# Optimization experiments

Hardware: AMD Instinct MI355X
Metric: run time of the kernel (lower is better)

Reference implementation:

```python
import jax, jax.numpy as jnp
from jax import lax
import numpy as np

B, T, F = 64, 2048, 256
H0, H1, O = 512, 512, 128


def setup_inputs() -> dict:
    key = jax.random.key(0)
    ks = jax.random.split(key, 16)
    s = lambda n: 1.0 / np.sqrt(n)
    return {
        "x": jax.random.normal(ks[0], (B, T, F), dtype=jnp.float32),
        # layer 0 RNN params (torch nn.RNN layout: W_ih [H,F], W_hh [H,H])
        "W_ih0": jax.random.uniform(ks[1], (H0, F), jnp.float32, -s(H0), s(H0)),
        "W_hh0": jax.random.uniform(ks[2], (H0, H0), jnp.float32, -s(H0), s(H0)),
        "b_ih0": jax.random.uniform(ks[3], (H0,), jnp.float32, -s(H0), s(H0)),
        "b_hh0": jax.random.uniform(ks[4], (H0,), jnp.float32, -s(H0), s(H0)),
        "h0_0": jax.random.normal(ks[5], (H0,), dtype=jnp.float32),  # buffer layer1 [1,1,H0]
        # layer 1 RNN params
        "W_ih1": jax.random.uniform(ks[6], (H1, H0), jnp.float32, -s(H1), s(H1)),
        "W_hh1": jax.random.uniform(ks[7], (H1, H1), jnp.float32, -s(H1), s(H1)),
        "b_ih1": jax.random.uniform(ks[8], (H1,), jnp.float32, -s(H1), s(H1)),
        "b_hh1": jax.random.uniform(ks[9], (H1,), jnp.float32, -s(H1), s(H1)),
        "h0_1": jax.random.normal(ks[10], (H1,), dtype=jnp.float32),  # buffer layer2 [1,1,H1]
        # final linear head
        "W_fc": jax.random.uniform(ks[11], (O, H1), jnp.float32, -s(H1), s(H1)),
        "b_fc": jax.random.uniform(ks[12], (O,), jnp.float32, -s(H1), s(H1)),
    }


def _rnn_layer(x, W_ih, W_hh, b_ih, b_hh, h0):
    # x: [B, T, Fin]; returns (outputs [B, T, H], last hidden [B, H])
    bs = x.shape[0]
    # precompute input projection as one big GEMM: [B, T, H]
    xp = jnp.einsum("btf,hf->bth", x, W_ih) + b_ih + b_hh
    h_init = jnp.broadcast_to(h0, (bs, h0.shape[0]))

    def step(h, xp_t):  # h: [B, H], xp_t: [B, H]
        h_new = jnp.tanh(xp_t + h @ W_hh.T)
        return h_new, h_new

    hT, hs = lax.scan(step, h_init, xp.transpose(1, 0, 2))  # time-major scan
    return hs.transpose(1, 0, 2), hT


def reference(x, W_ih0, W_hh0, b_ih0, b_hh0, h0_0,
              W_ih1, W_hh1, b_ih1, b_hh1, h0_1, W_fc, b_fc):
    res, _ = _rnn_layer(x, W_ih0, W_hh0, b_ih0, b_hh0, h0_0)
    _, hT = _rnn_layer(res, W_ih1, W_hh1, b_ih1, b_hh1, h0_1)
    # op[-1] is the last layer's final hidden state: [B, H1]
    return hT @ W_fc.T + b_fc  # [B, O]
```

## Files before the change

### kernel.cpp

```cpp
#include <hip/hip_runtime.h>

typedef _Float16 half_t;
typedef _Float16 f16x2 __attribute__((ext_vector_type(2)));
typedef _Float16 f16x8 __attribute__((ext_vector_type(8)));
typedef float f32x4 __attribute__((ext_vector_type(4)));

#define B_SZ 64
#define T_SZ 2048
#define F_SZ 256
#define H_SZ 512
#define O_SZ 128
#define NCH 32
#define CH 64

#if defined(__has_builtin)
#if __has_builtin(__builtin_amdgcn_fdot2)
#define HAS_FDOT2 1
#endif
#if __has_builtin(__builtin_amdgcn_rcpf)
#define HAS_RCPF 1
#endif
#endif
#ifndef HAS_FDOT2
#define HAS_FDOT2 0
#endif
#ifndef HAS_RCPF
#define HAS_RCPF 0
#endif

static __device__ __forceinline__ float fdot2(unsigned int w, unsigned int h, float acc) {
#if HAS_FDOT2
    return __builtin_amdgcn_fdot2(__builtin_bit_cast(f16x2, w), __builtin_bit_cast(f16x2, h), acc, false);
#else
    f16x2 wv = __builtin_bit_cast(f16x2, w);
    f16x2 hv = __builtin_bit_cast(f16x2, h);
    return acc + (float)wv[0] * (float)hv[0] + (float)wv[1] * (float)hv[1];
#endif
}

static __device__ __forceinline__ unsigned int pack_pair(float a, float b) {
    f16x2 p;
    p[0] = (half_t)a;
    p[1] = (half_t)b;
    return __builtin_bit_cast(unsigned int, p);
}

static __device__ __forceinline__ float fast_rcp(float x) {
#if HAS_RCPF
    return __builtin_amdgcn_rcpf(x);
#else
    return 1.0f / x;
#endif
}

static __device__ __forceinline__ void step_barrier() {
    __builtin_amdgcn_sched_barrier(0);
    asm volatile("s_waitcnt lgkmcnt(0)" ::: "memory");
    __builtin_amdgcn_s_barrier();
    __builtin_amdgcn_sched_barrier(0);
}


__global__ void cvt_f32_f16(const float* __restrict__ src, half_t* __restrict__ dst, int n) {
    int i = blockIdx.x * 256 + threadIdx.x;
    if (i < n) dst[i] = (half_t)src[i];
}

__global__ void zero_flags(unsigned int* __restrict__ p, int n) {
    int i = blockIdx.x * 256 + threadIdx.x;
    if (i < n) p[i] = 0u;
}

template<bool A_F32, int K>
__global__ __launch_bounds__(256) void gemm_xp(const void* __restrict__ Aptr,
                                               const half_t* __restrict__ Bw,
                                               const float* __restrict__ bias1,
                                               const float* __restrict__ bias2,
                                               half_t* __restrict__ Cout)
{
    const int nt   = blockIdx.x & 7;
    const int mt   = blockIdx.x >> 3;
    const int wave = threadIdx.x >> 6;
    const int lane = threadIdx.x & 63;
    const int mrow = mt * 64 + wave * 16 + (lane & 15);
    const int koff = (lane >> 4) * 8;

    f32x4 acc[4];
#pragma unroll
    for (int i = 0; i < 4; i++) acc[i] = (f32x4){0.f, 0.f, 0.f, 0.f};

#pragma unroll 2
    for (int k0 = 0; k0 < K; k0 += 32) {
        f16x8 a;
        if (A_F32) {
            const float* ap = (const float*)Aptr + (size_t)mrow * K + (k0 + koff);
            float4 v0 = ((const float4*)ap)[0];
            float4 v1 = ((const float4*)ap)[1];
            a[0] = (half_t)v0.x; a[1] = (half_t)v0.y; a[2] = (half_t)v0.z; a[3] = (half_t)v0.w;
            a[4] = (half_t)v1.x; a[5] = (half_t)v1.y; a[6] = (half_t)v1.z; a[7] = (half_t)v1.w;
        } else {
            const half_t* ap = (const half_t*)Aptr + (size_t)mrow * K + (k0 + koff);
            a = *(const f16x8*)ap;
        }
#pragma unroll
        for (int cb = 0; cb < 4; cb++) {
            const int col = nt * 64 + cb * 16 + (lane & 15);
            f16x8 bfrag = *(const f16x8*)(Bw + (size_t)col * K + (k0 + koff));
            acc[cb] = __builtin_amdgcn_mfma_f32_16x16x32_f16(a, bfrag, acc[cb], 0, 0, 0);
        }
    }
    const int rbase = mt * 64 + wave * 16 + (lane >> 4) * 4;
#pragma unroll
    for (int cb = 0; cb < 4; cb++) {
        const int col = nt * 64 + cb * 16 + (lane & 15);
        const float bsum = bias1[col] + bias2[col];
#pragma unroll
        for (int r = 0; r < 4; r++) {
            Cout[(size_t)(rbase + r) * H_SZ + col] = (half_t)(acc[cb][r] + bsum);
        }
    }
}

__global__ __launch_bounds__(512, 2)
void rnn_mega(half_t* bufA, half_t* bufB,
              const float* __restrict__ Whh0, const float* __restrict__ Whh1,
              const half_t* __restrict__ Wih1h,
              const float* __restrict__ h0_0, const float* __restrict__ h0_1,
              const float* __restrict__ b_ih1, const float* __restrict__ b_hh1,
              float* hT,
              unsigned int* flags0, unsigned int* flags1)
{
    __shared__ __align__(16) float part[2][8 * H_SZ];
    __shared__ __align__(16) uint4 wlds[12 * 512];
    __shared__ __align__(16) half_t hbuf[H_SZ];

    const int role = blockIdx.x % 3;
    const int b    = blockIdx.x / 3;
    const int tid  = threadIdx.x;
    const int l    = tid & 63;
    const int s    = tid >> 6;

    if (role == 1) {
        const int w = s, lane = l;
        const int koff = (lane >> 4) * 8;
        for (int chunk = 0; chunk < NCH; chunk++) {
            if (tid == 0) {
                while (__hip_atomic_load(&flags0[b * NCH + chunk], __ATOMIC_ACQUIRE,
                                         __HIP_MEMORY_SCOPE_AGENT) == 0u)
                    __builtin_amdgcn_s_sleep(2);
            }
            __syncthreads();
            const int t0 = chunk * CH;

            f32x4 gac[4][4];
#pragma unroll
            for (int rt = 0; rt < 4; rt++)
#pragma unroll
                for (int cb = 0; cb < 4; cb++) gac[rt][cb] = (f32x4){0.f, 0.f, 0.f, 0.f};

#pragma unroll 1
            for (int k0 = 0; k0 < H_SZ; k0 += 32) {
                f16x8 bf[4];
#pragma unroll
                for (int cb = 0; cb < 4; cb++)
                    bf[cb] = *(const f16x8*)(Wih1h +
                              (size_t)(64 * w + 16 * cb + (lane & 15)) * H_SZ + k0 + koff);
#pragma unroll
                for (int rt = 0; rt < 4; rt++) {
                    const f16x8 a = *(const f16x8*)((const half_t*)bufA +
                              ((size_t)b * T_SZ + t0 + rt * 16 + (lane & 15)) * H_SZ + k0 + koff);
#pragma unroll
                    for (int cb = 0; cb < 4; cb++)
                        gac[rt][cb] = __builtin_amdgcn_mfma_f32_16x16x32_f16(a, bf[cb], gac[rt][cb], 0, 0, 0);
                }
            }
#pragma unroll
            for (int rt = 0; rt < 4; rt++) {
                const int rbase = t0 + rt * 16 + (lane >> 4) * 4;
#pragma unroll
                for (int cb = 0; cb < 4; cb++) {
                    const int col = 64 * w + 16 * cb + (lane & 15);
                    const float bsum = b_ih1[col] + b_hh1[col];
#pragma unroll
                    for (int r = 0; r < 4; r++)
                        bufB[((size_t)b * T_SZ + rbase + r) * H_SZ + col] =
                            (half_t)(gac[rt][cb][r] + bsum);
                }
            }
            __syncthreads();
            if (tid == 0)
                __hip_atomic_store(&flags1[b * NCH + chunk], 1u, __ATOMIC_RELEASE,
                                   __HIP_MEMORY_SCOPE_AGENT);
        }
        return;
    }

    const bool L1 = (role == 2);
    const float* Whh = L1 ? Whh1 : Whh0;

    unsigned int wreg[208];
#pragma unroll
    for (int r = 0; r < 8; r++) {
        const float* wrow = Whh + (size_t)(8 * l + r) * H_SZ + 64 * s;
#pragma unroll
        for (int c = 0; c < 26; c++)
            wreg[c * 8 + r] = pack_pair(wrow[2 * c], wrow[2 * c + 1]);
    }
#pragma unroll
    for (int p2 = 0; p2 < 6; p2++) {
#pragma unroll
        for (int rh = 0; rh < 2; rh++) {
            unsigned int q[4];
#pragma unroll
            for (int rr = 0; rr < 4; rr++) {
                const int r = rh * 4 + rr;
                const float* wrow = Whh + (size_t)(8 * l + r) * H_SZ + 64 * s;
                const int c = 26 + p2;
                q[rr] = pack_pair(wrow[2 * c], wrow[2 * c + 1]);
            }
            uint4 v;
            v.x = q[0]; v.y = q[1]; v.z = q[2]; v.w = q[3];
            wlds[(p2 * 2 + rh) * 512 + tid] = v;
        }
    }
    hbuf[tid] = (half_t)((L1 ? h0_1 : h0_0)[tid]);
    __syncthreads();

    unsigned short* xp16 = (unsigned short*)(L1 ? bufB : bufA);
    const size_t base = (size_t)b * T_SZ * H_SZ + tid;

    const uint4* h16 = (const uint4*)(hbuf + 64 * s);
    const int x1     = (l >> 2) & 1;
    const int pslot0 = s * 128 + 2 * l + x1;
    const int pslot1 = s * 128 + 2 * l + (x1 ^ 1);
    const int fbase  = ((2 * (tid >> 3) + (((tid >> 2) & 1) ^ ((tid >> 5) & 1))) << 2) | (tid & 3);

#pragma unroll 1
    for (int chunk = 0; chunk < NCH; chunk++) {
        const int t0 = chunk * CH;
        if (L1) {
            if (tid == 0) {
                while (__hip_atomic_load(&flags1[b * NCH + chunk], __ATOMIC_ACQUIRE,
                                         __HIP_MEMORY_SCOPE_AGENT) == 0u)
                    __builtin_amdgcn_s_sleep(2);
            }
            __syncthreads();
        }
        unsigned short xpw_next = xp16[base + (size_t)t0 * H_SZ];

#pragma unroll 1
        for (int tt = 0; tt < CH; tt++) {
            const int t = t0 + tt;
            const unsigned short xpw = xpw_next;
            if (tt + 1 < CH) xpw_next = xp16[base + (size_t)(t + 1) * H_SZ];

            float acc[8];
#pragma unroll
            for (int r = 0; r < 8; r++) acc[r] = 0.f;

#pragma unroll
            for (int cc = 0; cc < 6; cc++) {
                const uint4 hv = h16[cc];
                const unsigned int hx0 = hv.x, hx1 = hv.y, hx2 = hv.z, hx3 = hv.w;
#pragma unroll
                for (int r = 0; r < 8; r++) acc[r] = fdot2(wreg[(cc * 4 + 0) * 8 + r], hx0, acc[r]);
#pragma unroll
                for (int r = 0; r < 8; r++) acc[r] = fdot2(wreg[(cc * 4 + 1) * 8 + r], hx1, acc[r]);
#pragma unroll
                for (int r = 0; r < 8; r++) acc[r] = fdot2(wreg[(cc * 4 + 2) * 8 + r], hx2, acc[r]);
#pragma unroll
                for (int r = 0; r < 8; r++) acc[r] = fdot2(wreg[(cc * 4 + 3) * 8 + r], hx3, acc[r]);
            }
#define LDSP(P2, H2) { \
                const uint4 w0 = wlds[((P2) * 2 + 0) * 512 + tid]; \
                const uint4 w1 = wlds[((P2) * 2 + 1) * 512 + tid]; \
                acc[0] = fdot2(w0.x, (H2), acc[0]); acc[1] = fdot2(w0.y, (H2), acc[1]); \
                acc[2] = fdot2(w0.z, (H2), acc[2]); acc[3] = fdot2(w0.w, (H2), acc[3]); \
                acc[4] = fdot2(w1.x, (H2), acc[4]); acc[5] = fdot2(w1.y, (H2), acc[5]); \
                acc[6] = fdot2(w1.z, (H2), acc[6]); acc[7] = fdot2(w1.w, (H2), acc[7]); }
            {
                const uint4 hv6 = h16[6];
#pragma unroll
                for (int r = 0; r < 8; r++) acc[r] = fdot2(wreg[24 * 8 + r], hv6.x, acc[r]);
#pragma unroll
                for (int r = 0; r < 8; r++) acc[r] = fdot2(wreg[25 * 8 + r], hv6.y, acc[r]);
                LDSP(0, hv6.z)
                LDSP(1, hv6.w)
                const uint4 hv7 = h16[7];
                LDSP(2, hv7.x)
                LDSP(3, hv7.y)
                LDSP(4, hv7.z)
                LDSP(5, hv7.w)
            }
#undef LDSP

            const int par = tt & 1;
            {
                float4* pb = (float4*)&part[par][0];
                float4 p0, p1;
                p0.x = acc[0]; p0.y = acc[1]; p0.z = acc[2]; p0.w = acc[3];
                p1.x = acc[4]; p1.y = acc[5]; p1.z = acc[6]; p1.w = acc[7];
                pb[pslot0] = p0;
                pb[pslot1] = p1;
            }
            step_barrier();

            float y;
            {
                half_t xv = __builtin_bit_cast(half_t, xpw);
                y = (float)xv;
            }
#pragma unroll
            for (int s2 = 0; s2 < 8; s2++) y += part[par][s2 * 512 + fbase];

            float e  = __expf(2.0f * y);
            float hn = 1.0f - 2.0f * fast_rcp(e + 1.0f);
            hbuf[tid] = (half_t)hn;
            if (!L1)
                xp16[base + (size_t)t * H_SZ] = __builtin_bit_cast(unsigned short, (half_t)hn);
            else if (t == T_SZ - 1)
                hT[(size_t)b * H_SZ + tid] = hn;
        }
        if (!L1) {
            __syncthreads();
            if (tid == 0)
                __hip_atomic_store(&flags0[b * NCH + chunk], 1u, __ATOMIC_RELEASE,
                                   __HIP_MEMORY_SCOPE_AGENT);
        }
    }
}

__global__ __launch_bounds__(128) void head_fc(const float* __restrict__ hT,
                                               const float* __restrict__ Wfc,
                                               const float* __restrict__ bfc,
                                               float* __restrict__ out)
{
    __shared__ float hs[H_SZ];
    const int b = blockIdx.x, o = threadIdx.x;
    for (int i = o; i < H_SZ; i += 128) hs[i] = hT[(size_t)b * H_SZ + i];
    __syncthreads();
    const float4* w4 = (const float4*)(Wfc + (size_t)o * H_SZ);
    const float4* h4 = (const float4*)hs;
    float acc = 0.f;
#pragma unroll 4
    for (int k = 0; k < H_SZ / 4; k++) {
        float4 w = w4[k], h = h4[k];
        acc += w.x * h.x + w.y * h.y + w.z * h.z + w.w * h.w;
    }
    out[(size_t)b * O_SZ + o] = acc + bfc[o];
}


extern "C" void kernel_launch(void* const* d_in, const int* in_sizes, int n_in,
                              void* d_out, int out_size, void* d_ws, size_t ws_size,
                              hipStream_t stream) {
    const float* x     = (const float*)d_in[0];
    const float* W_ih0 = (const float*)d_in[1];
    const float* W_hh0 = (const float*)d_in[2];
    const float* b_ih0 = (const float*)d_in[3];
    const float* b_hh0 = (const float*)d_in[4];
    const float* h0_0  = (const float*)d_in[5];
    const float* W_ih1 = (const float*)d_in[6];
    const float* W_hh1 = (const float*)d_in[7];
    const float* b_ih1 = (const float*)d_in[8];
    const float* b_hh1 = (const float*)d_in[9];
    const float* h0_1  = (const float*)d_in[10];
    const float* W_fc  = (const float*)d_in[11];
    const float* b_fc  = (const float*)d_in[12];

    char* ws = (char*)d_ws;
    size_t off = 0;
    const size_t bufElems = (size_t)B_SZ * T_SZ * H_SZ;
    half_t* bufA  = (half_t*)(ws + off); off += bufElems * 2;
    half_t* bufB  = (half_t*)(ws + off); off += bufElems * 2;
    half_t* Wih0h = (half_t*)(ws + off); off += (size_t)H_SZ * F_SZ * 2;
    half_t* Wih1h = (half_t*)(ws + off); off += (size_t)H_SZ * H_SZ * 2;
    float*  hTbuf = (float*)(ws + off);  off += (size_t)B_SZ * H_SZ * 4;
    const int FLAG_N = B_SZ * NCH;
    unsigned int* flags0 = (unsigned int*)(ws + off); off += (size_t)FLAG_N * 4;
    unsigned int* flags1 = (unsigned int*)(ws + off); off += (size_t)FLAG_N * 4;

    const int M = B_SZ * T_SZ;

    zero_flags<<<(2 * FLAG_N + 255) / 256, 256, 0, stream>>>(flags0, 2 * FLAG_N);
    cvt_f32_f16<<<(H_SZ * F_SZ + 255) / 256, 256, 0, stream>>>(W_ih0, Wih0h, H_SZ * F_SZ);
    cvt_f32_f16<<<(H_SZ * H_SZ + 255) / 256, 256, 0, stream>>>(W_ih1, Wih1h, H_SZ * H_SZ);

    gemm_xp<true, F_SZ><<<(M / 64) * 8, 256, 0, stream>>>(x, Wih0h, b_ih0, b_hh0, bufA);

    rnn_mega<<<192, 512, 0, stream>>>(bufA, bufB, W_hh0, W_hh1, Wih1h,
                                      h0_0, h0_1, b_ih1, b_hh1,
                                      hTbuf, flags0, flags1);

    head_fc<<<B_SZ, 128, 0, stream>>>(hTbuf, W_fc, b_fc, (float*)d_out);
}
```

Measured before the change: 4.081 ms.

## Replace LDS partial-sum reduction with intra-wave DPP reduction and double-buffered h

Each wave now owns 64 output rows, and the K dimension is split across the 8 lanes of each lane-group. Partial dot products are combined with three DPP adds followed by a select tree, instead of being written to LDS and summed after the barrier. The hidden state moves to a padded, double-buffered LDS array, which removes the need for the part buffer and leaves one barrier per step. The cost is extra DPP and select instructions, and h reads that are spread across lanes instead of broadcast.

```diff
diff --git a/kernel.cpp b/kernel.cpp
--- a/kernel.cpp
+++ b/kernel.cpp
@@ -51,6 +51,12 @@
 #else
     return 1.0f / x;
 #endif
+}
+
+template<int CTRL>
+static __device__ __forceinline__ float dpp_add(float x) {
+    int y = __builtin_amdgcn_mov_dpp(__builtin_bit_cast(int, x), CTRL, 0xF, 0xF, true);
+    return x + __builtin_bit_cast(float, y);
 }
 
 static __device__ __forceinline__ void step_barrier() {
@@ -130,9 +136,8 @@
               float* hT,
               unsigned int* flags0, unsigned int* flags1)
 {
-    __shared__ __align__(16) float part[2][8 * H_SZ];
     __shared__ __align__(16) uint4 wlds[12 * 512];
-    __shared__ __align__(16) half_t hbuf[H_SZ];
+    __shared__ __align__(16) half_t hpad[2][8 * 72];
 
     const int role = blockIdx.x % 3;
     const int b    = blockIdx.x / 3;
@@ -198,10 +203,13 @@
     const bool L1 = (role == 2);
     const float* Whh = L1 ? Whh1 : Whh0;
 
+    const int q  = l >> 3;
+    const int sp = l & 7;
+
     unsigned int wreg[208];
 #pragma unroll
     for (int r = 0; r < 8; r++) {
-        const float* wrow = Whh + (size_t)(8 * l + r) * H_SZ + 64 * s;
+        const float* wrow = Whh + (size_t)(64 * s + 8 * q + r) * H_SZ + 64 * sp;
 #pragma unroll
         for (int c = 0; c < 26; c++)
             wreg[c * 8 + r] = pack_pair(wrow[2 * c], wrow[2 * c + 1]);
@@ -210,30 +218,33 @@
     for (int p2 = 0; p2 < 6; p2++) {
 #pragma unroll
         for (int rh = 0; rh < 2; rh++) {
-            unsigned int q[4];
+            unsigned int qv[4];
 #pragma unroll
             for (int rr = 0; rr < 4; rr++) {
                 const int r = rh * 4 + rr;
-                const float* wrow = Whh + (size_t)(8 * l + r) * H_SZ + 64 * s;
+                const float* wrow = Whh + (size_t)(64 * s + 8 * q + r) * H_SZ + 64 * sp;
                 const int c = 26 + p2;
-                q[rr] = pack_pair(wrow[2 * c], wrow[2 * c + 1]);
+                qv[rr] = pack_pair(wrow[2 * c], wrow[2 * c + 1]);
             }
             uint4 v;
-            v.x = q[0]; v.y = q[1]; v.z = q[2]; v.w = q[3];
+            v.x = qv[0]; v.y = qv[1]; v.z = qv[2]; v.w = qv[3];
             wlds[(p2 * 2 + rh) * 512 + tid] = v;
         }
     }
-    hbuf[tid] = (half_t)((L1 ? h0_1 : h0_0)[tid]);
+    hpad[0][s * 72 + l] = (half_t)((L1 ? h0_1 : h0_0)[tid]);
     __syncthreads();
 
     unsigned short* xp16 = (unsigned short*)(L1 ? bufB : bufA);
     const size_t base = (size_t)b * T_SZ * H_SZ + tid;
 
-    const uint4* h16 = (const uint4*)(hbuf + 64 * s);
-    const int x1     = (l >> 2) & 1;
-    const int pslot0 = s * 128 + 2 * l + x1;
-    const int pslot1 = s * 128 + 2 * l + (x1 ^ 1);
-    const int fbase  = ((2 * (tid >> 3) + (((tid >> 2) & 1) ^ ((tid >> 5) & 1))) << 2) | (tid & 3);
+    const uint4* hp0 = (const uint4*)(&hpad[0][sp * 72]);
+    const uint4* hp1 = (const uint4*)(&hpad[1][sp * 72]);
+    half_t* hw0 = &hpad[0][s * 72 + l];
+    half_t* hw1 = &hpad[1][s * 72 + l];
+
+    const bool sb0 = (sp & 1) != 0;
+    const bool sb1 = (sp & 2) != 0;
+    const bool sb2 = (sp & 4) != 0;
 
 #pragma unroll 1
     for (int chunk = 0; chunk < NCH; chunk++) {
@@ -251,6 +262,7 @@
 #pragma unroll 1
         for (int tt = 0; tt < CH; tt++) {
             const int t = t0 + tt;
+            const int par = tt & 1;
             const unsigned short xpw = xpw_next;
             if (tt + 1 < CH) xpw_next = xp16[base + (size_t)(t + 1) * H_SZ];
 
@@ -258,9 +270,11 @@
 #pragma unroll
             for (int r = 0; r < 8; r++) acc[r] = 0.f;
 
+            const uint4* hp = par ? hp1 : hp0;
+
 #pragma unroll
             for (int cc = 0; cc < 6; cc++) {
-                const uint4 hv = h16[cc];
+                const uint4 hv = hp[cc];
                 const unsigned int hx0 = hv.x, hx1 = hv.y, hx2 = hv.z, hx3 = hv.w;
 #pragma unroll
                 for (int r = 0; r < 8; r++) acc[r] = fdot2(wreg[(cc * 4 + 0) * 8 + r], hx0, acc[r]);
@@ -279,14 +293,14 @@
                 acc[4] = fdot2(w1.x, (H2), acc[4]); acc[5] = fdot2(w1.y, (H2), acc[5]); \
                 acc[6] = fdot2(w1.z, (H2), acc[6]); acc[7] = fdot2(w1.w, (H2), acc[7]); }
             {
-                const uint4 hv6 = h16[6];
+                const uint4 hv6 = hp[6];
 #pragma unroll
                 for (int r = 0; r < 8; r++) acc[r] = fdot2(wreg[24 * 8 + r], hv6.x, acc[r]);
 #pragma unroll
                 for (int r = 0; r < 8; r++) acc[r] = fdot2(wreg[25 * 8 + r], hv6.y, acc[r]);
                 LDSP(0, hv6.z)
                 LDSP(1, hv6.w)
-                const uint4 hv7 = h16[7];
+                const uint4 hv7 = hp[7];
                 LDSP(2, hv7.x)
                 LDSP(3, hv7.y)
                 LDSP(4, hv7.z)
@@ -294,32 +308,37 @@
             }
 #undef LDSP
 
-            const int par = tt & 1;
-            {
-                float4* pb = (float4*)&part[par][0];
-                float4 p0, p1;
-                p0.x = acc[0]; p0.y = acc[1]; p0.z = acc[2]; p0.w = acc[3];
-                p1.x = acc[4]; p1.y = acc[5]; p1.z = acc[6]; p1.w = acc[7];
-                pb[pslot0] = p0;
-                pb[pslot1] = p1;
-            }
-            step_barrier();
+#pragma unroll
+            for (int r = 0; r < 8; r++) {
+                float a = acc[r];
+                a = dpp_add<0x0B1>(a);
+                a = dpp_add<0x04E>(a);
+                a = dpp_add<0x141>(a);
+                acc[r] = a;
+            }
+            float t0s = sb0 ? acc[1] : acc[0];
+            float t1s = sb0 ? acc[3] : acc[2];
+            float t2s = sb0 ? acc[5] : acc[4];
+            float t3s = sb0 ? acc[7] : acc[6];
+            float u0s = sb1 ? t1s : t0s;
+            float u1s = sb1 ? t3s : t2s;
+            float rsum = sb2 ? u1s : u0s;
 
             float y;
             {
                 half_t xv = __builtin_bit_cast(half_t, xpw);
-                y = (float)xv;
-            }
-#pragma unroll
-            for (int s2 = 0; s2 < 8; s2++) y += part[par][s2 * 512 + fbase];
-
+                y = (float)xv + rsum;
+            }
             float e  = __expf(2.0f * y);
             float hn = 1.0f - 2.0f * fast_rcp(e + 1.0f);
-            hbuf[tid] = (half_t)hn;
+
+            *(par ? hw0 : hw1) = (half_t)hn;
             if (!L1)
                 xp16[base + (size_t)t * H_SZ] = __builtin_bit_cast(unsigned short, (half_t)hn);
             else if (t == T_SZ - 1)
                 hT[(size_t)b * H_SZ + tid] = hn;
+
+            step_barrier();
         }
         if (!L1) {
             __syncthreads();
```

After: 3.638 ms. 1.12x faster.

## Compute recurrent matvec with MFMA per wave and drop cross-wave partial reduction

Applied to the files above, without the earlier changes.

Each wave now computes a contiguous block of 64 hidden outputs over the full K=512 using 16x16x32 f16 MFMA instructions. The hidden vector is replicated across the A-operand rows, and W_hh stays resident in registers with an LDS spill. Previously each wave produced partial sums over a K-slice with fdot2, wrote them to LDS and reduced them after a barrier. The new code double-buffers hbuf so each timestep needs only one barrier, and it drops the partial-sum LDS traffic and reduction. In exchange, 15/16 of the MFMA rows are redundant work and the per-step dependency chain becomes 16 MFMAs per accumulator.

```diff
diff --git a/kernel.cpp b/kernel.cpp
--- a/kernel.cpp
+++ b/kernel.cpp
@@ -14,36 +14,13 @@
 #define CH 64
 
 #if defined(__has_builtin)
-#if __has_builtin(__builtin_amdgcn_fdot2)
-#define HAS_FDOT2 1
-#endif
 #if __has_builtin(__builtin_amdgcn_rcpf)
 #define HAS_RCPF 1
 #endif
 #endif
-#ifndef HAS_FDOT2
-#define HAS_FDOT2 0
-#endif
 #ifndef HAS_RCPF
 #define HAS_RCPF 0
 #endif
-
-static __device__ __forceinline__ float fdot2(unsigned int w, unsigned int h, float acc) {
-#if HAS_FDOT2
-    return __builtin_amdgcn_fdot2(__builtin_bit_cast(f16x2, w), __builtin_bit_cast(f16x2, h), acc, false);
-#else
-    f16x2 wv = __builtin_bit_cast(f16x2, w);
-    f16x2 hv = __builtin_bit_cast(f16x2, h);
-    return acc + (float)wv[0] * (float)hv[0] + (float)wv[1] * (float)hv[1];
-#endif
-}
-
-static __device__ __forceinline__ unsigned int pack_pair(float a, float b) {
-    f16x2 p;
-    p[0] = (half_t)a;
-    p[1] = (half_t)b;
-    return __builtin_bit_cast(unsigned int, p);
-}
 
 static __device__ __forceinline__ float fast_rcp(float x) {
 #if HAS_RCPF
@@ -130,9 +107,8 @@
               float* hT,
               unsigned int* flags0, unsigned int* flags1)
 {
-    __shared__ __align__(16) float part[2][8 * H_SZ];
-    __shared__ __align__(16) uint4 wlds[12 * 512];
-    __shared__ __align__(16) half_t hbuf[H_SZ];
+    __shared__ __align__(16) uint4  wlds[12 * 512];
+    __shared__ __align__(16) half_t hbuf[2][H_SZ];
 
     const int role = blockIdx.x % 3;
     const int b    = blockIdx.x / 3;
@@ -198,42 +174,37 @@
     const bool L1 = (role == 2);
     const float* Whh = L1 ? Whh1 : Whh0;
 
-    unsigned int wreg[208];
-#pragma unroll
-    for (int r = 0; r < 8; r++) {
-        const float* wrow = Whh + (size_t)(8 * l + r) * H_SZ + 64 * s;
-#pragma unroll
-        for (int c = 0; c < 26; c++)
-            wreg[c * 8 + r] = pack_pair(wrow[2 * c], wrow[2 * c + 1]);
-    }
-#pragma unroll
-    for (int p2 = 0; p2 < 6; p2++) {
-#pragma unroll
-        for (int rh = 0; rh < 2; rh++) {
-            unsigned int q[4];
-#pragma unroll
-            for (int rr = 0; rr < 4; rr++) {
-                const int r = rh * 4 + rr;
-                const float* wrow = Whh + (size_t)(8 * l + r) * H_SZ + 64 * s;
-                const int c = 26 + p2;
-                q[rr] = pack_pair(wrow[2 * c], wrow[2 * c + 1]);
-            }
-            uint4 v;
-            v.x = q[0]; v.y = q[1]; v.z = q[2]; v.w = q[3];
-            wlds[(p2 * 2 + rh) * 512 + tid] = v;
-        }
-    }
-    hbuf[tid] = (half_t)((L1 ? h0_1 : h0_0)[tid]);
+    const int n15 = l & 15;
+    const int kg  = l >> 4;
+
+    f16x8 breg[13][4];
+#pragma unroll
+    for (int kt = 0; kt < 13; kt++) {
+#pragma unroll
+        for (int n = 0; n < 4; n++) {
+            const float* wr = Whh + (size_t)(64 * s + 16 * n + n15) * H_SZ + 32 * kt + 8 * kg;
+            f16x8 f;
+#pragma unroll
+            for (int j = 0; j < 8; j++) f[j] = (half_t)wr[j];
+            breg[kt][n] = f;
+        }
+    }
+#pragma unroll
+    for (int kt2 = 0; kt2 < 3; kt2++) {
+#pragma unroll
+        for (int n = 0; n < 4; n++) {
+            const float* wr = Whh + (size_t)(64 * s + 16 * n + n15) * H_SZ + 32 * (13 + kt2) + 8 * kg;
+            f16x8 f;
+#pragma unroll
+            for (int j = 0; j < 8; j++) f[j] = (half_t)wr[j];
+            wlds[(kt2 * 4 + n) * 512 + tid] = __builtin_bit_cast(uint4, f);
+        }
+    }
+    hbuf[0][tid] = (half_t)((L1 ? h0_1 : h0_0)[tid]);
     __syncthreads();
 
     unsigned short* xp16 = (unsigned short*)(L1 ? bufB : bufA);
     const size_t base = (size_t)b * T_SZ * H_SZ + tid;
-
-    const uint4* h16 = (const uint4*)(hbuf + 64 * s);
-    const int x1     = (l >> 2) & 1;
-    const int pslot0 = s * 128 + 2 * l + x1;
-    const int pslot1 = s * 128 + 2 * l + (x1 ^ 1);
-    const int fbase  = ((2 * (tid >> 3) + (((tid >> 2) & 1) ^ ((tid >> 5) & 1))) << 2) | (tid & 3);
 
 #pragma unroll 1
     for (int chunk = 0; chunk < NCH; chunk++) {
@@ -251,75 +222,49 @@
 #pragma unroll 1
         for (int tt = 0; tt < CH; tt++) {
             const int t = t0 + tt;
+            const int par = tt & 1;
             const unsigned short xpw = xpw_next;
             if (tt + 1 < CH) xpw_next = xp16[base + (size_t)(t + 1) * H_SZ];
 
-            float acc[8];
-#pragma unroll
-            for (int r = 0; r < 8; r++) acc[r] = 0.f;
-
-#pragma unroll
-            for (int cc = 0; cc < 6; cc++) {
-                const uint4 hv = h16[cc];
-                const unsigned int hx0 = hv.x, hx1 = hv.y, hx2 = hv.z, hx3 = hv.w;
-#pragma unroll
-                for (int r = 0; r < 8; r++) acc[r] = fdot2(wreg[(cc * 4 + 0) * 8 + r], hx0, acc[r]);
-#pragma unroll
-                for (int r = 0; r < 8; r++) acc[r] = fdot2(wreg[(cc * 4 + 1) * 8 + r], hx1, acc[r]);
-#pragma unroll
-                for (int r = 0; r < 8; r++) acc[r] = fdot2(wreg[(cc * 4 + 2) * 8 + r], hx2, acc[r]);
-#pragma unroll
-                for (int r = 0; r < 8; r++) acc[r] = fdot2(wreg[(cc * 4 + 3) * 8 + r], hx3, acc[r]);
-            }
-#define LDSP(P2, H2) { \
-                const uint4 w0 = wlds[((P2) * 2 + 0) * 512 + tid]; \
-                const uint4 w1 = wlds[((P2) * 2 + 1) * 512 + tid]; \
-                acc[0] = fdot2(w0.x, (H2), acc[0]); acc[1] = fdot2(w0.y, (H2), acc[1]); \
-                acc[2] = fdot2(w0.z, (H2), acc[2]); acc[3] = fdot2(w0.w, (H2), acc[3]); \
-                acc[4] = fdot2(w1.x, (H2), acc[4]); acc[5] = fdot2(w1.y, (H2), acc[5]); \
-                acc[6] = fdot2(w1.z, (H2), acc[6]); acc[7] = fdot2(w1.w, (H2), acc[7]); }
-            {
-                const uint4 hv6 = h16[6];
-#pragma unroll
-                for (int r = 0; r < 8; r++) acc[r] = fdot2(wreg[24 * 8 + r], hv6.x, acc[r]);
-#pragma unroll
-                for (int r = 0; r < 8; r++) acc[r] = fdot2(wreg[25 * 8 + r], hv6.y, acc[r]);
-                LDSP(0, hv6.z)
-                LDSP(1, hv6.w)
-                const uint4 hv7 = h16[7];
-                LDSP(2, hv7.x)
-                LDSP(3, hv7.y)
-                LDSP(4, hv7.z)
-                LDSP(5, hv7.w)
-            }
-#undef LDSP
-
-            const int par = tt & 1;
-            {
-                float4* pb = (float4*)&part[par][0];
-                float4 p0, p1;
-                p0.x = acc[0]; p0.y = acc[1]; p0.z = acc[2]; p0.w = acc[3];
-                p1.x = acc[4]; p1.y = acc[5]; p1.z = acc[6]; p1.w = acc[7];
-                pb[pslot0] = p0;
-                pb[pslot1] = p1;
-            }
+            const half_t* hc_ = hbuf[par];
+
+            f32x4 acc[4];
+#pragma unroll
+            for (int n = 0; n < 4; n++) acc[n] = (f32x4){0.f, 0.f, 0.f, 0.f};
+
+#pragma unroll
+            for (int kt = 0; kt < 13; kt++) {
+                const f16x8 a = *(const f16x8*)(hc_ + 32 * kt + 8 * kg);
+#pragma unroll
+                for (int n = 0; n < 4; n++)
+                    acc[n] = __builtin_amdgcn_mfma_f32_16x16x32_f16(a, breg[kt][n], acc[n], 0, 0, 0);
+            }
+#pragma unroll
+            for (int kt2 = 0; kt2 < 3; kt2++) {
+                const f16x8 a = *(const f16x8*)(hc_ + 32 * (13 + kt2) + 8 * kg);
+#pragma unroll
+                for (int n = 0; n < 4; n++) {
+                    const f16x8 bf = __builtin_bit_cast(f16x8, wlds[(kt2 * 4 + n) * 512 + tid]);
+                    acc[n] = __builtin_amdgcn_mfma_f32_16x16x32_f16(a, bf, acc[n], 0, 0, 0);
+                }
+            }
+
+            float va   = (kg & 1) ? acc[1][0] : acc[0][0];
+            float vb   = (kg & 1) ? acc[3][0] : acc[2][0];
+            float rsum = (kg & 2) ? vb : va;
+
+            half_t xv = __builtin_bit_cast(half_t, xpw);
+            float y   = (float)xv + rsum;
+            float e2  = __expf(2.0f * y);
+            float hn2 = 1.0f - 2.0f * fast_rcp(e2 + 1.0f);
+
+            hbuf[par ^ 1][tid] = (half_t)hn2;
+            if (!L1)
+                xp16[base + (size_t)t * H_SZ] = __builtin_bit_cast(unsigned short, (half_t)hn2);
+            else if (t == T_SZ - 1)
+                hT[(size_t)b * H_SZ + tid] = hn2;
+
             step_barrier();
-
-            float y;
-            {
-                half_t xv = __builtin_bit_cast(half_t, xpw);
-                y = (float)xv;
-            }
-#pragma unroll
-            for (int s2 = 0; s2 < 8; s2++) y += part[par][s2 * 512 + fbase];
-
-            float e  = __expf(2.0f * y);
-            float hn = 1.0f - 2.0f * fast_rcp(e + 1.0f);
-            hbuf[tid] = (half_t)hn;
-            if (!L1)
-                xp16[base + (size_t)t * H_SZ] = __builtin_bit_cast(unsigned short, (half_t)hn);
-            else if (t == T_SZ - 1)
-                hT[(size_t)b * H_SZ + tid] = hn;
         }
         if (!L1) {
             __syncthreads();
```

New measurement: 3.906 ms. -4.3%, faster.
